# Kernel tuning notes

Hardware: AMD Instinct MI355X
Metric: run time of the kernel (lower is better)

The kernel has to match this reference:

```python
import jax, jax.numpy as jnp
import numpy as np
from jax import lax

BN_EPS = 1e-5
DN = ('NCHW', 'OIHW', 'NCHW')


def _bn_silu(y, s, b, m, v):
    # eval-mode BatchNorm2d followed by SiLU
    inv = s / jnp.sqrt(v + BN_EPS)
    y = y * inv[None, :, None, None] + (b - m * inv)[None, :, None, None]
    return jax.nn.silu(y)


def _dsconv(x, dw_w, pw_w, s, b, m, v):
    c = x.shape[1]
    y = lax.conv_general_dilated(x, dw_w, (1, 1), [(1, 1), (1, 1)],
                                 dimension_numbers=DN, feature_group_count=c)
    y = lax.conv_general_dilated(y, pw_w, (1, 1), [(0, 0), (0, 0)],
                                 dimension_numbers=DN)
    return _bn_silu(y, s, b, m, v)


def setup_inputs() -> dict:
    key = jax.random.key(0)
    ks = jax.random.split(key, 8)
    B, C, H, W, OUT, TOPK = 32, 256, 64, 64, 256, 2
    CS = C // 2
    inp = {
        'x': jax.random.normal(ks[0], (B, C, H, W), jnp.float32),
        'weights': jax.random.uniform(ks[1], (B, TOPK), jnp.float32),
        'indices': jax.random.randint(ks[2], (B, TOPK), 0, 4),
        'dw_w0': jax.random.normal(ks[3], (CS, 1, 3, 3), jnp.float32) * 0.1,
        'pw_w0': jax.random.normal(ks[4], (OUT, CS, 1, 1), jnp.float32) * 0.05,
        'bn0_s': jnp.ones((OUT,), jnp.float32),
        'bn0_b': jnp.zeros((OUT,), jnp.float32),
        'bn0_m': jnp.zeros((OUT,), jnp.float32),
        'bn0_v': jnp.ones((OUT,), jnp.float32),
        'dw_w1': jax.random.normal(ks[5], (CS, 1, 3, 3), jnp.float32) * 0.1,
        'pw_w1': jax.random.normal(ks[6], (OUT, CS, 1, 1), jnp.float32) * 0.05,
        'bn1_s': jnp.ones((OUT,), jnp.float32),
        'bn1_b': jnp.zeros((OUT,), jnp.float32),
        'bn1_m': jnp.zeros((OUT,), jnp.float32),
        'bn1_v': jnp.ones((OUT,), jnp.float32),
        'w2': jax.random.normal(ks[7], (OUT, C, 1, 1), jnp.float32) * 0.05,
        'bn2_s': jnp.ones((OUT,), jnp.float32),
        'bn2_b': jnp.zeros((OUT,), jnp.float32),
        'bn2_m': jnp.zeros((OUT,), jnp.float32),
        'bn2_v': jnp.ones((OUT,), jnp.float32),
    }
    return inp


def reference(x, weights, indices,
              dw_w0, pw_w0, bn0_s, bn0_b, bn0_m, bn0_v,
              dw_w1, pw_w1, bn1_s, bn1_b, bn1_m, bn1_v,
              w2, bn2_s, bn2_b, bn2_m, bn2_v):
    cs = x.shape[1] // 2
    x_rgb, x_ir = x[:, :cs], x[:, cs:]
    # Per-expert routing coefficient: sum over top-k slots of weight * (index == e).
    # Mathematically identical to the torch masked scatter-add loop.
    def coeff(e):
        return jnp.sum(weights * (indices == e).astype(weights.dtype), axis=1)  # [B]
    e0 = _dsconv(x_rgb, dw_w0, pw_w0, bn0_s, bn0_b, bn0_m, bn0_v)
    e1 = _dsconv(x_ir, dw_w1, pw_w1, bn1_s, bn1_b, bn1_m, bn1_v)
    e2 = _bn_silu(lax.conv_general_dilated(x, w2, (1, 1), [(0, 0), (0, 0)],
                                           dimension_numbers=DN),
                  bn2_s, bn2_b, bn2_m, bn2_v)
    out = (coeff(0)[:, None, None, None] * e0
           + coeff(1)[:, None, None, None] * e1
           + coeff(2)[:, None, None, None] * e2)
    return out
```

## Files before the change

kernel.cpp:

```cpp
#include <hip/hip_runtime.h>

typedef __bf16 bf16x8 __attribute__((ext_vector_type(8)));
typedef float f32x4 __attribute__((ext_vector_type(4)));

#define BN_EPS 1e-5f

__device__ __forceinline__ unsigned short f2bf(float f) {
    union { float f; unsigned u; } x; x.f = f;
    unsigned r = x.u + 0x7fffu + ((x.u >> 16) & 1u);
    return (unsigned short)(r >> 16);
}

__device__ __forceinline__ unsigned pk_bf16(float lo, float hi) {
    unsigned r;
    asm("v_cvt_pk_bf16_f32 %0, %1, %2" : "=v"(r) : "v"(lo), "v"(hi));
    return r;
}

__global__ void prep_kernel(const float* __restrict__ pw0, const float* __restrict__ pw1,
                            const float* __restrict__ w2,
                            const float* __restrict__ s0, const float* __restrict__ b0,
                            const float* __restrict__ m0, const float* __restrict__ v0,
                            const float* __restrict__ s1, const float* __restrict__ b1,
                            const float* __restrict__ m1, const float* __restrict__ v1,
                            const float* __restrict__ s2, const float* __restrict__ b2,
                            const float* __restrict__ m2, const float* __restrict__ v2,
                            unsigned short* __restrict__ wfF0, unsigned short* __restrict__ wfF1,
                            unsigned short* __restrict__ wfF2, float* __restrict__ beta) {
    int o = blockIdx.x;
    int t = threadIdx.x;
    float inv0 = s0[o] * rsqrtf(v0[o] + BN_EPS);
    float inv1 = s1[o] * rsqrtf(v1[o] + BN_EPS);
    float inv2 = s2[o] * rsqrtf(v2[o] + BN_EPS);
    if (t == 0) {
        beta[0 * 256 + o] = b0[o] - m0[o] * inv0;
        beta[1 * 256 + o] = b1[o] - m1[o] * inv1;
        beta[2 * 256 + o] = b2[o] - m2[o] * inv2;
    }
    if (t < 128) {
        wfF0[((t >> 3) * 256 + o) * 8 + (t & 7)] = f2bf(pw0[o * 128 + t] * inv0);
        wfF1[((t >> 3) * 256 + o) * 8 + (t & 7)] = f2bf(pw1[o * 128 + t] * inv1);
    }
    wfF2[((t >> 3) * 256 + o) * 8 + (t & 7)] = f2bf(w2[o * 256 + t] * inv2);
}

template<int NK>
__device__ __forceinline__ void gemm_expert(const char* lds, const unsigned short* __restrict__ W,
                                            int qb, int wave, int l15, int l4,
                                            const int* pxv, const int* swv, f32x4 acc[2][4]) {
    const int row0 = wave * 32 + l15;
    bf16x8 aC[2], bC[4];
#pragma unroll
    for (int ot = 0; ot < 2; ++ot)
        aC[ot] = *(const bf16x8*)(W + (l4 * 256 + row0 + ot * 16) * 8);
#pragma unroll
    for (int tp = 0; tp < 4; ++tp)
        bC[tp] = *(const bf16x8*)(lds + pxv[tp] * 512 + ((qb + l4 * 16) ^ swv[tp]));

#pragma unroll
    for (int kk = 0; kk < NK; ++kk) {
        bf16x8 aN[2], bN[4];
        if (kk + 1 < NK) {
#pragma unroll
            for (int ot = 0; ot < 2; ++ot)
                aN[ot] = *(const bf16x8*)(W + (((kk + 1) * 4 + l4) * 256 + row0 + ot * 16) * 8);
#pragma unroll
            for (int tp = 0; tp < 4; ++tp)
                bN[tp] = *(const bf16x8*)(lds + pxv[tp] * 512 + ((qb + (kk + 1) * 64 + l4 * 16) ^ swv[tp]));
        }
#pragma unroll
        for (int ot = 0; ot < 2; ++ot)
#pragma unroll
            for (int tp = 0; tp < 4; ++tp)
                acc[ot][tp] = __builtin_amdgcn_mfma_f32_16x16x32_bf16(aC[ot], bC[tp], acc[ot][tp], 0, 0, 0);
        if (kk + 1 < NK) {
#pragma unroll
            for (int ot = 0; ot < 2; ++ot) aC[ot] = aN[ot];
#pragma unroll
            for (int tp = 0; tp < 4; ++tp) bC[tp] = bN[tp];
        }
    }
}

__device__ __forceinline__ void epilogue(const f32x4 acc[2][4], float ce, const float* __restrict__ bp,
                                         int wave, int l4, f32x4 res[2][4]) {
#pragma unroll
    for (int ot = 0; ot < 2; ++ot)
#pragma unroll
        for (int j = 0; j < 4; ++j) {
            const int o = wave * 32 + ot * 16 + l4 * 4 + j;
            const float bet = bp[o];
#pragma unroll
            for (int tp = 0; tp < 4; ++tp) {
                float v = acc[ot][tp][j] + bet;
                float sig = __builtin_amdgcn_rcpf(1.f + __expf(-v));
                res[ot][tp][j] += ce * (v * sig);
            }
        }
}

__global__ __launch_bounds__(512, 4)
void fused_kernel(const float* __restrict__ x,
                  const float* __restrict__ wts, const int* __restrict__ idx,
                  const float* __restrict__ dw0, const float* __restrict__ dw1,
                  const unsigned short* __restrict__ wfF0,
                  const unsigned short* __restrict__ wfF1,
                  const unsigned short* __restrict__ wfF2,
                  const float* __restrict__ beta,
                  float* __restrict__ out) {
    __shared__ __align__(16) char lds[34816];

    const int tid  = threadIdx.x;
    const int wave = tid >> 6;
    const int lane = tid & 63;

    const int bid = blockIdx.x;
    const int nb  = ((bid & 7) << 8) | (bid >> 3);
    const int b   = nb >> 6;
    const int h   = nb & 63;

    float c0 = 0.f, c1 = 0.f, c2 = 0.f;
#pragma unroll
    for (int t = 0; t < 2; ++t) {
        int e = idx[b * 2 + t];
        float w = wts[b * 2 + t];
        if (e == 0) c0 += w;
        else if (e == 1) c1 += w;
        else if (e == 2) c2 += w;
    }
    const bool do0 = (c0 != 0.f), do1 = (c1 != 0.f), do2 = (c2 != 0.f);

    const long rowBase = (long)b * 1048576L;

    const int g   = lane >> 2;
    const int kq  = lane & 3;
    const int px0 = g * 4;
    const int l15 = lane & 15;
    const int l4  = lane >> 4;
    const float* xb = x + rowBase + h * 64 + px0;
    const bool hm = (h > 0), hp = (h < 63);

    f32x4 res[2][4];
#pragma unroll
    for (int ot = 0; ot < 2; ++ot)
#pragma unroll
        for (int tp = 0; tp < 4; ++tp)
            res[ot][tp] = (f32x4){0.f, 0.f, 0.f, 0.f};

    int pxv[4], swv[4];
#pragma unroll
    for (int tp = 0; tp < 4; ++tp) {
        pxv[tp] = tp * 16 + l15;
        swv[tp] = (pxv[tp] & 15) << 4;
    }

    if (do0 || do1) {
        if ((wave < 4) ? do0 : do1) {
#pragma unroll
            for (int i = 0; i < 2; ++i) {
                const int k0 = wave * 32 + i * 16 + kq * 4;
                unsigned dw_p[2][4];
#pragma unroll
                for (int pr = 0; pr < 2; ++pr) {
                    float y[2][4];
#pragma unroll
                    for (int k2 = 0; k2 < 2; ++k2) {
                        const int k = k0 + pr * 2 + k2;
                        const float* dwp = (k < 128) ? (dw0 + k * 9) : (dw1 + (k - 128) * 9);
                        const float* xc = xb + (long)k * 4096;
                        float4 rm = hm ? *(const float4*)(xc - 64) : make_float4(0.f, 0.f, 0.f, 0.f);
                        float4 rc = *(const float4*)(xc);
                        float4 rp = hp ? *(const float4*)(xc + 64) : make_float4(0.f, 0.f, 0.f, 0.f);
                        float lm = __shfl_up(rm.w, 4), lc = __shfl_up(rc.w, 4), lp = __shfl_up(rp.w, 4);
                        float Rm = __shfl_down(rm.x, 4), Rc = __shfl_down(rc.x, 4), Rp = __shfl_down(rp.x, 4);
                        if (g == 0)  { lm = 0.f; lc = 0.f; lp = 0.f; }
                        if (g == 15) { Rm = 0.f; Rc = 0.f; Rp = 0.f; }
                        const float w0 = dwp[0], w1 = dwp[1], w2 = dwp[2];
                        const float w3 = dwp[3], w4 = dwp[4], w5 = dwp[5];
                        const float w6 = dwp[6], w7 = dwp[7], w8 = dwp[8];
                        y[k2][0] = w0*lm   + w1*rm.x + w2*rm.y + w3*lc   + w4*rc.x + w5*rc.y + w6*lp   + w7*rp.x + w8*rp.y;
                        y[k2][1] = w0*rm.x + w1*rm.y + w2*rm.z + w3*rc.x + w4*rc.y + w5*rc.z + w6*rp.x + w7*rp.y + w8*rp.z;
                        y[k2][2] = w0*rm.y + w1*rm.z + w2*rm.w + w3*rc.y + w4*rc.z + w5*rc.w + w6*rp.y + w7*rp.z + w8*rp.w;
                        y[k2][3] = w0*rm.z + w1*rm.w + w2*Rm   + w3*rc.z + w4*rc.w + w5*Rc   + w6*rp.z + w7*rp.w + w8*Rp;
                    }
#pragma unroll
                    for (int j = 0; j < 4; ++j)
                        dw_p[pr][j] = pk_bf16(y[0][j], y[1][j]);
                }
                const int colb = (k0 >> 3) * 16;
                const int sub  = (k0 & 4) * 2;
#pragma unroll
                for (int j = 0; j < 4; ++j) {
                    const int px = px0 + j;
                    *(uint2*)(lds + px * 512 + ((colb ^ ((px & 15) << 4))) + sub) =
                        make_uint2(dw_p[0][j], dw_p[1][j]);
                }
            }
        }
        __syncthreads();
        if (do0) {
            f32x4 acc[2][4];
#pragma unroll
            for (int ot = 0; ot < 2; ++ot)
#pragma unroll
                for (int tp = 0; tp < 4; ++tp) acc[ot][tp] = (f32x4){0.f, 0.f, 0.f, 0.f};
            gemm_expert<4>(lds, wfF0, 0, wave, l15, l4, pxv, swv, acc);
            epilogue(acc, c0, beta, wave, l4, res);
        }
        if (do1) {
            f32x4 acc[2][4];
#pragma unroll
            for (int ot = 0; ot < 2; ++ot)
#pragma unroll
                for (int tp = 0; tp < 4; ++tp) acc[ot][tp] = (f32x4){0.f, 0.f, 0.f, 0.f};
            gemm_expert<4>(lds, wfF1, 256, wave, l15, l4, pxv, swv, acc);
            epilogue(acc, c1, beta + 256, wave, l4, res);
        }
    }

    if (do2) {
        __syncthreads();
        {
            const int cb = wave * 32 + kq * 8;
            float4 r[8];
#pragma unroll
            for (int c = 0; c < 8; ++c)
                r[c] = *(const float4*)(xb + (long)(cb + c) * 4096);
            const int colb = (cb >> 3) * 16;
#pragma unroll
            for (int j = 0; j < 4; ++j) {
                const int px = px0 + j;
                float v0 = (j == 0) ? r[0].x : (j == 1) ? r[0].y : (j == 2) ? r[0].z : r[0].w;
                float v1 = (j == 0) ? r[1].x : (j == 1) ? r[1].y : (j == 2) ? r[1].z : r[1].w;
                float v2 = (j == 0) ? r[2].x : (j == 1) ? r[2].y : (j == 2) ? r[2].z : r[2].w;
                float v3 = (j == 0) ? r[3].x : (j == 1) ? r[3].y : (j == 2) ? r[3].z : r[3].w;
                float v4 = (j == 0) ? r[4].x : (j == 1) ? r[4].y : (j == 2) ? r[4].z : r[4].w;
                float v5 = (j == 0) ? r[5].x : (j == 1) ? r[5].y : (j == 2) ? r[5].z : r[5].w;
                float v6 = (j == 0) ? r[6].x : (j == 1) ? r[6].y : (j == 2) ? r[6].z : r[6].w;
                float v7 = (j == 0) ? r[7].x : (j == 1) ? r[7].y : (j == 2) ? r[7].z : r[7].w;
                *(uint4*)(lds + px * 512 + ((colb ^ ((px & 15) << 4)))) =
                    make_uint4(pk_bf16(v0, v1), pk_bf16(v2, v3), pk_bf16(v4, v5), pk_bf16(v6, v7));
            }
        }
        __syncthreads();
        {
            f32x4 acc[2][4];
#pragma unroll
            for (int ot = 0; ot < 2; ++ot)
#pragma unroll
                for (int tp = 0; tp < 4; ++tp) acc[ot][tp] = (f32x4){0.f, 0.f, 0.f, 0.f};
            gemm_expert<8>(lds, wfF2, 0, wave, l15, l4, pxv, swv, acc);
            epilogue(acc, c2, beta + 512, wave, l4, res);
        }
    }

    float* lf = (float*)lds;
    const long outB = rowBase + h * 64;
    __syncthreads();
#pragma unroll
    for (int r = 0; r < 2; ++r) {
        if ((wave >> 2) == r) {
#pragma unroll
            for (int ot = 0; ot < 2; ++ot)
#pragma unroll
                for (int j = 0; j < 4; ++j) {
                    const int o = wave * 32 + ot * 16 + l4 * 4 + j;
#pragma unroll
                    for (int tp = 0; tp < 4; ++tp)
                        lf[(o & 127) * 68 + tp * 16 + l15] = res[ot][tp][j];
                }
        }
        __syncthreads();
        {
            const int rowq = tid >> 3;
            const int col  = (tid & 7) * 8;
#pragma unroll
            for (int rr = 0; rr < 2; ++rr) {
                const int lr = rowq + rr * 64;
                float4 v0 = *(float4*)&lf[lr * 68 + col];
                float4 v1 = *(float4*)&lf[lr * 68 + col + 4];
                float* op = out + outB + (long)(r * 128 + lr) * 4096 + col;
                *(float4*)op = v0;
                *(float4*)(op + 4) = v1;
            }
        }
        __syncthreads();
    }
}

extern "C" void kernel_launch(void* const* d_in, const int* in_sizes, int n_in,
                              void* d_out, int out_size, void* d_ws, size_t ws_size,
                              hipStream_t stream) {
    const float* x    = (const float*)d_in[0];
    const float* wts  = (const float*)d_in[1];
    const int*   idx  = (const int*)d_in[2];
    const float* dw0  = (const float*)d_in[3];
    const float* pw0  = (const float*)d_in[4];
    const float* s0   = (const float*)d_in[5];
    const float* b0   = (const float*)d_in[6];
    const float* m0   = (const float*)d_in[7];
    const float* v0   = (const float*)d_in[8];
    const float* dw1  = (const float*)d_in[9];
    const float* pw1  = (const float*)d_in[10];
    const float* s1   = (const float*)d_in[11];
    const float* b1   = (const float*)d_in[12];
    const float* m1   = (const float*)d_in[13];
    const float* v1   = (const float*)d_in[14];
    const float* w2   = (const float*)d_in[15];
    const float* s2   = (const float*)d_in[16];
    const float* b2   = (const float*)d_in[17];
    const float* m2   = (const float*)d_in[18];
    const float* v2   = (const float*)d_in[19];

    char* ws = (char*)d_ws;
    unsigned short* wfF0 = (unsigned short*)ws;
    unsigned short* wfF1 = (unsigned short*)(ws + 65536);
    unsigned short* wfF2 = (unsigned short*)(ws + 131072);
    float*          beta = (float*)(ws + 262144);

    prep_kernel<<<256, 256, 0, stream>>>(pw0, pw1, w2,
                                         s0, b0, m0, v0,
                                         s1, b1, m1, v1,
                                         s2, b2, m2, v2,
                                         wfF0, wfF1, wfF2, beta);

    fused_kernel<<<2048, 512, 0, stream>>>(x, wts, idx, dw0, dw1,
                                           wfF0, wfF1, wfF2, beta, (float*)d_out);
}
```

Measured before the change: 92.36 us.

## Share x loads between depthwise and dense paths, single-pass output staging

The x center-row float4 loaded for the depthwise conv is also packed to bf16 and written to a second LDS region (offset 32768) for the dense expert, so the separate re-read of x and its two barriers are gone. LDS doubles to 68 KB, which lets the output transpose stage all 256 channels at once instead of in two passes with extra barriers. The cost is higher LDS usage per block, which may lower occupancy under launch_bounds(512,4).

Measured after the change: 93.52 us. No clear change (+1.3%).

```diff
diff --git a/kernel.cpp b/kernel.cpp
--- a/kernel.cpp
+++ b/kernel.cpp
@@ -15,6 +15,10 @@
     unsigned r;
     asm("v_cvt_pk_bf16_f32 %0, %1, %2" : "=v"(r) : "v"(lo), "v"(hi));
     return r;
+}
+
+__device__ __forceinline__ float fcomp(float4 v, int j) {
+    return (j == 0) ? v.x : (j == 1) ? v.y : (j == 2) ? v.z : v.w;
 }
 
 __global__ void prep_kernel(const float* __restrict__ pw0, const float* __restrict__ pw1,
@@ -108,7 +112,7 @@
                   const unsigned short* __restrict__ wfF2,
                   const float* __restrict__ beta,
                   float* __restrict__ out) {
-    __shared__ __align__(16) char lds[34816];
+    __shared__ __align__(16) char lds[69632];
 
     const int tid  = threadIdx.x;
     const int wave = tid >> 6;
@@ -154,22 +158,25 @@
         swv[tp] = (pxv[tp] & 15) << 4;
     }
 
-    if (do0 || do1) {
-        if ((wave < 4) ? do0 : do1) {
-#pragma unroll
-            for (int i = 0; i < 2; ++i) {
-                const int k0 = wave * 32 + i * 16 + kq * 4;
-                unsigned dw_p[2][4];
-#pragma unroll
-                for (int pr = 0; pr < 2; ++pr) {
-                    float y[2][4];
-#pragma unroll
-                    for (int k2 = 0; k2 < 2; ++k2) {
-                        const int k = k0 + pr * 2 + k2;
+    const bool dwact = (wave < 4) ? do0 : do1;
+    if (dwact || do2) {
+#pragma unroll
+        for (int i = 0; i < 2; ++i) {
+            const int k0 = wave * 32 + i * 16 + kq * 4;
+            unsigned dw_p[2][4], rw_p[2][4];
+#pragma unroll
+            for (int pr = 0; pr < 2; ++pr) {
+                float y[2][4];
+                float4 rcv[2];
+#pragma unroll
+                for (int k2 = 0; k2 < 2; ++k2) {
+                    const int k = k0 + pr * 2 + k2;
+                    const float* xc = xb + (long)k * 4096;
+                    float4 rc = *(const float4*)(xc);
+                    rcv[k2] = rc;
+                    if (dwact) {
                         const float* dwp = (k < 128) ? (dw0 + k * 9) : (dw1 + (k - 128) * 9);
-                        const float* xc = xb + (long)k * 4096;
                         float4 rm = hm ? *(const float4*)(xc - 64) : make_float4(0.f, 0.f, 0.f, 0.f);
-                        float4 rc = *(const float4*)(xc);
                         float4 rp = hp ? *(const float4*)(xc + 64) : make_float4(0.f, 0.f, 0.f, 0.f);
                         float lm = __shfl_up(rm.w, 4), lc = __shfl_up(rc.w, 4), lp = __shfl_up(rp.w, 4);
                         float Rm = __shfl_down(rm.x, 4), Rc = __shfl_down(rc.x, 4), Rp = __shfl_down(rp.x, 4);
@@ -183,108 +190,91 @@
                         y[k2][2] = w0*rm.y + w1*rm.z + w2*rm.w + w3*rc.y + w4*rc.z + w5*rc.w + w6*rp.y + w7*rp.z + w8*rp.w;
                         y[k2][3] = w0*rm.z + w1*rm.w + w2*Rm   + w3*rc.z + w4*rc.w + w5*Rc   + w6*rp.z + w7*rp.w + w8*Rp;
                     }
+                }
+                if (dwact) {
 #pragma unroll
                     for (int j = 0; j < 4; ++j)
                         dw_p[pr][j] = pk_bf16(y[0][j], y[1][j]);
                 }
-                const int colb = (k0 >> 3) * 16;
-                const int sub  = (k0 & 4) * 2;
-#pragma unroll
-                for (int j = 0; j < 4; ++j) {
-                    const int px = px0 + j;
-                    *(uint2*)(lds + px * 512 + ((colb ^ ((px & 15) << 4))) + sub) =
-                        make_uint2(dw_p[0][j], dw_p[1][j]);
+                if (do2) {
+#pragma unroll
+                    for (int j = 0; j < 4; ++j)
+                        rw_p[pr][j] = pk_bf16(fcomp(rcv[0], j), fcomp(rcv[1], j));
                 }
             }
-        }
-        __syncthreads();
-        if (do0) {
-            f32x4 acc[2][4];
-#pragma unroll
-            for (int ot = 0; ot < 2; ++ot)
-#pragma unroll
-                for (int tp = 0; tp < 4; ++tp) acc[ot][tp] = (f32x4){0.f, 0.f, 0.f, 0.f};
-            gemm_expert<4>(lds, wfF0, 0, wave, l15, l4, pxv, swv, acc);
-            epilogue(acc, c0, beta, wave, l4, res);
-        }
-        if (do1) {
-            f32x4 acc[2][4];
-#pragma unroll
-            for (int ot = 0; ot < 2; ++ot)
-#pragma unroll
-                for (int tp = 0; tp < 4; ++tp) acc[ot][tp] = (f32x4){0.f, 0.f, 0.f, 0.f};
-            gemm_expert<4>(lds, wfF1, 256, wave, l15, l4, pxv, swv, acc);
-            epilogue(acc, c1, beta + 256, wave, l4, res);
-        }
-    }
-
+            const int colb = (k0 >> 3) * 16;
+            const int sub  = (k0 & 4) * 2;
+#pragma unroll
+            for (int j = 0; j < 4; ++j) {
+                const int px  = px0 + j;
+                const int off = px * 512 + ((colb ^ ((px & 15) << 4))) + sub;
+                if (dwact)
+                    *(uint2*)(lds + off) = make_uint2(dw_p[0][j], dw_p[1][j]);
+                if (do2)
+                    *(uint2*)(lds + 32768 + off) = make_uint2(rw_p[0][j], rw_p[1][j]);
+            }
+        }
+    }
+    __syncthreads();
+
+    if (do0) {
+        f32x4 acc[2][4];
+#pragma unroll
+        for (int ot = 0; ot < 2; ++ot)
+#pragma unroll
+            for (int tp = 0; tp < 4; ++tp) acc[ot][tp] = (f32x4){0.f, 0.f, 0.f, 0.f};
+        gemm_expert<4>(lds, wfF0, 0, wave, l15, l4, pxv, swv, acc);
+        epilogue(acc, c0, beta, wave, l4, res);
+    }
+    if (do1) {
+        f32x4 acc[2][4];
+#pragma unroll
+        for (int ot = 0; ot < 2; ++ot)
+#pragma unroll
+            for (int tp = 0; tp < 4; ++tp) acc[ot][tp] = (f32x4){0.f, 0.f, 0.f, 0.f};
+        gemm_expert<4>(lds, wfF1, 256, wave, l15, l4, pxv, swv, acc);
+        epilogue(acc, c1, beta + 256, wave, l4, res);
+    }
     if (do2) {
-        __syncthreads();
-        {
-            const int cb = wave * 32 + kq * 8;
-            float4 r[8];
-#pragma unroll
-            for (int c = 0; c < 8; ++c)
-                r[c] = *(const float4*)(xb + (long)(cb + c) * 4096);
-            const int colb = (cb >> 3) * 16;
-#pragma unroll
-            for (int j = 0; j < 4; ++j) {
-                const int px = px0 + j;
-                float v0 = (j == 0) ? r[0].x : (j == 1) ? r[0].y : (j == 2) ? r[0].z : r[0].w;
-                float v1 = (j == 0) ? r[1].x : (j == 1) ? r[1].y : (j == 2) ? r[1].z : r[1].w;
-                float v2 = (j == 0) ? r[2].x : (j == 1) ? r[2].y : (j == 2) ? r[2].z : r[2].w;
-                float v3 = (j == 0) ? r[3].x : (j == 1) ? r[3].y : (j == 2) ? r[3].z : r[3].w;
-                float v4 = (j == 0) ? r[4].x : (j == 1) ? r[4].y : (j == 2) ? r[4].z : r[4].w;
-                float v5 = (j == 0) ? r[5].x : (j == 1) ? r[5].y : (j == 2) ? r[5].z : r[5].w;
-                float v6 = (j == 0) ? r[6].x : (j == 1) ? r[6].y : (j == 2) ? r[6].z : r[6].w;
-                float v7 = (j == 0) ? r[7].x : (j == 1) ? r[7].y : (j == 2) ? r[7].z : r[7].w;
-                *(uint4*)(lds + px * 512 + ((colb ^ ((px & 15) << 4)))) =
-                    make_uint4(pk_bf16(v0, v1), pk_bf16(v2, v3), pk_bf16(v4, v5), pk_bf16(v6, v7));
-            }
-        }
-        __syncthreads();
-        {
-            f32x4 acc[2][4];
-#pragma unroll
-            for (int ot = 0; ot < 2; ++ot)
-#pragma unroll
-                for (int tp = 0; tp < 4; ++tp) acc[ot][tp] = (f32x4){0.f, 0.f, 0.f, 0.f};
-            gemm_expert<8>(lds, wfF2, 0, wave, l15, l4, pxv, swv, acc);
-            epilogue(acc, c2, beta + 512, wave, l4, res);
-        }
+        f32x4 acc[2][4];
+#pragma unroll
+        for (int ot = 0; ot < 2; ++ot)
+#pragma unroll
+            for (int tp = 0; tp < 4; ++tp) acc[ot][tp] = (f32x4){0.f, 0.f, 0.f, 0.f};
+        gemm_expert<8>(lds + 32768, wfF2, 0, wave, l15, l4, pxv, swv, acc);
+        epilogue(acc, c2, beta + 512, wave, l4, res);
     }
 
     float* lf = (float*)lds;
     const long outB = rowBase + h * 64;
     __syncthreads();
-#pragma unroll
-    for (int r = 0; r < 2; ++r) {
-        if ((wave >> 2) == r) {
-#pragma unroll
-            for (int ot = 0; ot < 2; ++ot)
-#pragma unroll
-                for (int j = 0; j < 4; ++j) {
-                    const int o = wave * 32 + ot * 16 + l4 * 4 + j;
-#pragma unroll
-                    for (int tp = 0; tp < 4; ++tp)
-                        lf[(o & 127) * 68 + tp * 16 + l15] = res[ot][tp][j];
-                }
-        }
-        __syncthreads();
-        {
-            const int rowq = tid >> 3;
-            const int col  = (tid & 7) * 8;
-#pragma unroll
-            for (int rr = 0; rr < 2; ++rr) {
-                const int lr = rowq + rr * 64;
-                float4 v0 = *(float4*)&lf[lr * 68 + col];
-                float4 v1 = *(float4*)&lf[lr * 68 + col + 4];
-                float* op = out + outB + (long)(r * 128 + lr) * 4096 + col;
-                *(float4*)op = v0;
-                *(float4*)(op + 4) = v1;
+    {
+        const int reg  = wave >> 2;
+        const int rbase = reg * 8704;
+#pragma unroll
+        for (int ot = 0; ot < 2; ++ot)
+#pragma unroll
+            for (int j = 0; j < 4; ++j) {
+                const int row = (wave & 3) * 32 + ot * 16 + l4 * 4 + j;
+#pragma unroll
+                for (int tp = 0; tp < 4; ++tp)
+                    lf[rbase + row * 68 + tp * 16 + l15] = res[ot][tp][j];
             }
-        }
-        __syncthreads();
+    }
+    __syncthreads();
+    {
+        const int rowq = tid >> 3;
+        const int col  = (tid & 7) * 8;
+#pragma unroll
+        for (int rr = 0; rr < 4; ++rr) {
+            const int lr = rowq + rr * 64;
+            const int ad = (lr >> 7) * 8704 + (lr & 127) * 68 + col;
+            float4 v0 = *(float4*)&lf[ad];
+            float4 v1 = *(float4*)&lf[ad + 4];
+            float* op = out + outB + (long)lr * 4096 + col;
+            *(float4*)op = v0;
+            *(float4*)(op + 4) = v1;
+        }
     }
 }
 
```
